# Kernel optimization log

Measured on AMD Instinct MI355X. Metric: run time of the kernel, lower is better.

The kernel has to match this reference:

```python
import jax, jax.numpy as jnp
import numpy as np
from jax import lax

# Mamba2 hyperparameters (mamba_ssm defaults scaled to d_model=512)
D_MODEL = 512
EXPAND = 2
D_INNER = EXPAND * D_MODEL          # 1024
HEADDIM = 64
NHEADS = D_INNER // HEADDIM         # 16
D_STATE = 64
NGROUPS = 1
D_CONV = 4
CONV_DIM = D_INNER + 2 * NGROUPS * D_STATE   # 1152
D_IN_PROJ = 2 * D_INNER + 2 * NGROUPS * D_STATE + NHEADS  # 2192
EPS = 1e-5


def setup_inputs() -> dict:
    key = jax.random.key(0)
    ks = jax.random.split(key, 8)
    x = jax.random.normal(ks[0], (4, 2044, D_MODEL), jnp.float32)
    in_proj_w = jax.random.normal(ks[1], (D_MODEL, D_IN_PROJ), jnp.float32) * 0.02
    conv_w = jax.random.normal(ks[2], (CONV_DIM, 1, D_CONV), jnp.float32) * 0.2  # depthwise [O,I/g,K]
    conv_b = jnp.zeros((CONV_DIM,), jnp.float32)
    dt_bias = jax.random.uniform(ks[3], (NHEADS,), jnp.float32, 0.0, 0.1)
    A_log = jnp.log(jax.random.uniform(ks[4], (NHEADS,), jnp.float32, 1.0, 16.0))
    D_skip = jnp.ones((NHEADS,), jnp.float32)
    norm_w = jnp.ones((D_INNER,), jnp.float32)
    out_proj_w = jax.random.normal(ks[5], (D_INNER, D_MODEL), jnp.float32) * 0.02
    return {
        "x": x, "in_proj_w": in_proj_w, "conv_w": conv_w, "conv_b": conv_b,
        "dt_bias": dt_bias, "A_log": A_log, "D_skip": D_skip,
        "norm_w": norm_w, "out_proj_w": out_proj_w,
    }


def _mamba2(x, in_proj_w, conv_w, conv_b, dt_bias, A_log, D_skip, norm_w, out_proj_w):
    B, Lp, _ = x.shape
    zxbcdt = x @ in_proj_w                                  # [B,Lp,D_IN_PROJ]
    z = zxbcdt[..., :D_INNER]                               # gate
    xBC = zxbcdt[..., D_INNER:D_INNER + CONV_DIM]
    dt = zxbcdt[..., D_INNER + CONV_DIM:]                   # [B,Lp,H]

    # causal depthwise conv over time, then silu
    xBC_c = lax.conv_general_dilated(
        xBC.transpose(0, 2, 1), conv_w, window_strides=(1,),
        padding=[(D_CONV - 1, 0)], feature_group_count=CONV_DIM,
        dimension_numbers=("NCH", "OIH", "NCH"))
    xBC = jax.nn.silu(xBC_c.transpose(0, 2, 1) + conv_b)    # [B,Lp,CONV_DIM]

    xs = xBC[..., :D_INNER]
    Bm = xBC[..., D_INNER:D_INNER + NGROUPS * D_STATE]      # [B,Lp,N] (g=1)
    Cm = xBC[..., D_INNER + NGROUPS * D_STATE:]             # [B,Lp,N]

    dt = jax.nn.softplus(dt + dt_bias)                      # [B,Lp,H]
    A = -jnp.exp(A_log)                                     # [H]
    xh = xs.reshape(B, Lp, NHEADS, HEADDIM)                 # [B,Lp,H,P]

    decay = jnp.exp(dt * A)                                 # [B,Lp,H]
    dtx = dt[..., None] * xh                                # [B,Lp,H,P]

    def step(h, inp):
        dec_t, dtx_t, B_t, C_t = inp                        # [B,H],[B,H,P],[B,N],[B,N]
        h = dec_t[:, :, None, None] * h + dtx_t[..., None] * B_t[:, None, None, :]
        y_t = jnp.einsum("bhpn,bn->bhp", h, C_t)
        return h, y_t

    h0 = jnp.zeros((B, NHEADS, HEADDIM, D_STATE), x.dtype)
    _, ys = lax.scan(step, h0, (decay.transpose(1, 0, 2),
                                dtx.transpose(1, 0, 2, 3),
                                Bm.transpose(1, 0, 2),
                                Cm.transpose(1, 0, 2)))
    y = ys.transpose(1, 0, 2, 3) + D_skip[None, None, :, None] * xh  # [B,Lp,H,P]
    y = y.reshape(B, Lp, D_INNER)

    # gated RMSNorm (RMSNormGated): gate first, then normalize
    y = y * jax.nn.silu(z)
    y = y * lax.rsqrt(jnp.mean(y * y, axis=-1, keepdims=True) + EPS) * norm_w
    return y @ out_proj_w                                   # [B,Lp,D_MODEL]


def reference(x, in_proj_w, conv_w, conv_b, dt_bias, A_log, D_skip, norm_w, out_proj_w):
    # MemoryEfficientMamba wrapper: pad seq_len to multiple of 8, run mamba, slice back
    L = x.shape[1]
    pad = (-L) % 8
    xp = jnp.pad(x, ((0, 0), (0, pad), (0, 0))) if pad else x
    out = _mamba2(xp, in_proj_w, conv_w, conv_b, dt_bias, A_log, D_skip, norm_w, out_proj_w)
    return out[:, :L, :]
```

## Files before the change

kernel.cpp:

```cpp
#include <hip/hip_runtime.h>
#include <hip/hip_bf16.h>
#include <math.h>
#include <string.h>

#define BATCH   4
#define SEQ     2044
#define DMODEL  512
#define DINNER  1024
#define NHEADS  16
#define HEADDIM 64
#define DSTATE  64
#define CONVDIM 1152
#define DINPROJ 2192
#define ZW      2176
#define NROWS   (BATCH*SEQ)
#define Q       64
#define NCHUNK  32

typedef __attribute__((ext_vector_type(8))) short bf16x8;
typedef __attribute__((ext_vector_type(4))) float f32x4;

#define MFMA(a,b,c) __builtin_amdgcn_mfma_f32_16x16x32_bf16((a),(b),(c),0,0,0)

__device__ inline short f2bf(float f) {
    __hip_bfloat16 h = __float2bfloat16(f);
    short s; memcpy(&s, &h, 2); return s;
}
__device__ inline float bf2f(short s) {
    unsigned u = ((unsigned)(unsigned short)s) << 16;
    float f; memcpy(&f, &u, 4); return f;
}

__device__ __forceinline__ void gload16(const short* g, short* l) {
    __builtin_amdgcn_global_load_lds(
        (const __attribute__((address_space(1))) void*)g,
        (__attribute__((address_space(3))) void*)l, 16, 0, 0);
}

__global__ __launch_bounds__(256) void convert_bf16_kernel(const float* __restrict__ in,
                                                           short* __restrict__ out, int n8) {
    int i = blockIdx.x * 256 + threadIdx.x;
    if (i >= n8) return;
    float4 v0 = *((const float4*)in + i * 2);
    float4 v1 = *((const float4*)in + i * 2 + 1);
    short t[8];
    t[0]=f2bf(v0.x); t[1]=f2bf(v0.y); t[2]=f2bf(v0.z); t[3]=f2bf(v0.w);
    t[4]=f2bf(v1.x); t[5]=f2bf(v1.y); t[6]=f2bf(v1.z); t[7]=f2bf(v1.w);
    *((bf16x8*)out + i) = *(const bf16x8*)t;
}

__global__ __launch_bounds__(256) void transpose_cvt_kernel(const float* __restrict__ in,
                                                            short* __restrict__ out,
                                                            int R, int Cc, int ldi) {
    __shared__ float tile[64][65];
    const int bx = blockIdx.x * 64;
    const int by = blockIdx.y * 64;
    const int tid = threadIdx.x;
#pragma unroll
    for (int i = 0; i < 16; i++) {
        int idx = tid + i * 256; int r = idx >> 6, c = idx & 63;
        float v = 0.f;
        if (by + r < R && bx + c < Cc) v = in[(size_t)(by + r) * ldi + bx + c];
        tile[r][c] = v;
    }
    __syncthreads();
#pragma unroll
    for (int i = 0; i < 16; i++) {
        int idx = tid + i * 256; int c = idx >> 6, r = idx & 63;
        if (bx + c < Cc && by + r < R)
            out[(size_t)(bx + c) * R + by + r] = f2bf(tile[r][c]);
    }
}

template<bool BF16OUT>
__global__ __launch_bounds__(256) void gemm_bf16(const short* __restrict__ A,
                                                 const short* __restrict__ Bt,
                                                 void* __restrict__ Cv,
                                                 int M, int N, int K,
                                                 int Nbf, float* __restrict__ dtout,
                                                 const float* __restrict__ dt_bias,
                                                 const float* __restrict__ A_log) {
    __shared__ short As[2][64][64];
    __shared__ short Bs[2][64][64];
    const int tid = threadIdx.x;
    const int wave = tid >> 6, lane = tid & 63;
    const int bm = blockIdx.x * 64, bn = blockIdx.y * 64;
    const int lane15 = lane & 15;
    const int kgrp = lane >> 4;
    const int srow = lane >> 3;
    const int scol = (lane & 7) ^ srow;
    const int r7 = lane15 & 7;

    f32x4 acc[4];
#pragma unroll
    for (int j = 0; j < 4; j++) acc[j] = (f32x4){0.f, 0.f, 0.f, 0.f};

    const short* Ab = A + (size_t)(bm + wave * 16 + srow) * K + scol * 8;
    const short* Bb = Bt + (size_t)(bn + wave * 16 + srow) * K + scol * 8;

    gload16(Ab,                 &As[0][wave * 16][0]);
    gload16(Ab + 8 * (size_t)K, &As[0][wave * 16 + 8][0]);
    gload16(Bb,                 &Bs[0][wave * 16][0]);
    gload16(Bb + 8 * (size_t)K, &Bs[0][wave * 16 + 8][0]);
    __syncthreads();

    const int nk = K >> 6;
    int cur = 0;
    for (int s = 0; s < nk; s++) {
        if (s + 1 < nk) {
            const int kk = (s + 1) << 6;
            const int nxt = cur ^ 1;
            gload16(Ab + kk,                 &As[nxt][wave * 16][0]);
            gload16(Ab + 8 * (size_t)K + kk, &As[nxt][wave * 16 + 8][0]);
            gload16(Bb + kk,                 &Bs[nxt][wave * 16][0]);
            gload16(Bb + 8 * (size_t)K + kk, &Bs[nxt][wave * 16 + 8][0]);
        }
        const int arow = (wave << 4) + lane15;
        bf16x8 a0 = *(const bf16x8*)&As[cur][arow][(kgrp ^ r7) * 8];
        bf16x8 a1 = *(const bf16x8*)&As[cur][arow][((kgrp + 4) ^ r7) * 8];
#pragma unroll
        for (int j = 0; j < 4; j++) {
            const int brow = (j << 4) + lane15;
            bf16x8 b0 = *(const bf16x8*)&Bs[cur][brow][(kgrp ^ r7) * 8];
            bf16x8 b1 = *(const bf16x8*)&Bs[cur][brow][((kgrp + 4) ^ r7) * 8];
            acc[j] = MFMA(a0, b0, acc[j]);
            acc[j] = MFMA(a1, b1, acc[j]);
        }
        __syncthreads();
        cur ^= 1;
    }

    const int crow = bm + (wave << 4) + ((lane >> 4) << 2);
    const int ccol0 = bn + lane15;
    const int ndt = N - Nbf;
#pragma unroll
    for (int j = 0; j < 4; j++) {
        int gn = ccol0 + j * 16;
        if (gn >= N) continue;
#pragma unroll
        for (int i = 0; i < 4; i++) {
            int gm = crow + i;
            if (gm >= M) continue;
            float v = acc[j][i];
            if (BF16OUT) {
                if (dtout != nullptr && gn >= Nbf) {
                    int h = gn - Nbf;
                    float v2 = v + dt_bias[h];
                    float sp = (v2 > 20.f) ? v2 : log1pf(expf(v2));
                    dtout[(size_t)gm * ndt + h] = sp * (-expf(A_log[h]));
                } else {
                    ((short*)Cv)[(size_t)gm * Nbf + gn] = f2bf(v);
                }
            } else {
                ((float*)Cv)[(size_t)gm * N + gn] = v;
            }
        }
    }
}

__global__ __launch_bounds__(256) void conv_silu_kernel(const short* __restrict__ zxb,
                                                        const float* __restrict__ conv_w,
                                                        const float* __restrict__ conv_b,
                                                        short* __restrict__ convo) {
    int idx = blockIdx.x * 256 + threadIdx.x;
    if (idx >= BATCH * (SEQ/4) * CONVDIM) return;
    int c = idx % CONVDIM;
    int q = idx / CONVDIM;
    int b = q / (SEQ/4);
    int t0 = (q % (SEQ/4)) * 4;
    const size_t base = ((size_t)b * SEQ + t0) * ZW + DINNER + c;
    float4 wv = *(const float4*)&conv_w[c * 4];
    float xv[7];
#pragma unroll
    for (int i = 0; i < 7; i++) {
        int t = t0 - 3 + i;
        xv[i] = (t >= 0) ? bf2f(zxb[base + (size_t)(i - 3) * ZW]) : 0.f;
    }
    const float bias = conv_b[c];
    const size_t obase = ((size_t)b * SEQ + t0) * CONVDIM + c;
#pragma unroll
    for (int i = 0; i < 4; i++) {
        float a = bias + xv[i]*wv.x + xv[i+1]*wv.y + xv[i+2]*wv.z + xv[i+3]*wv.w;
        float s = a / (1.f + expf(-a));
        convo[obase + (size_t)i * CONVDIM] = f2bf(s);
    }
}

__global__ __launch_bounds__(256) void chunk_state_kernel(
    const short* __restrict__ convo,
    const float* __restrict__ lab,
    const float* __restrict__ A_log,
    short* __restrict__ Sbf,
    float* __restrict__ atot)
{
    const int blk = blockIdx.x;
    const int h  = blk & 15;
    const int bc = blk >> 4;
    const int c  = bc & (NCHUNK - 1);
    const int b  = bc >> 5;
    const int t0 = c * Q;
    const int len = min(Q, SEQ - t0);
    const int tid = threadIdx.x;
    const int wave = tid >> 6, lane = tid & 63;
    const size_t rowbase = (size_t)b * SEQ + t0;

    __shared__ short Xt[64][72];
    __shared__ short Bw[64][72];
    __shared__ float sw[64];

    if (tid < 64) {
        const float nAinv = -expf(-A_log[h]);
        float lav = 0.f;
        if (tid < len) lav = lab[(rowbase + tid) * NHEADS + h];
        float dtv = lav * nAinv;
        float v = lav;
#pragma unroll
        for (int off = 1; off < 64; off <<= 1) {
            float nb = __shfl_up(v, off);
            if (lane >= off) v += nb;
        }
        float last = __shfl(v, 63);
        sw[tid] = expf(last - v) * dtv;
        if (tid == 63) atot[blk] = expf(last);
    }
    __syncthreads();

    {
        const int r = tid >> 2, qq = tid & 3;
        const bf16x8 zz = {0,0,0,0,0,0,0,0};
        bf16x8 b0 = zz, b1 = zz, x0 = zz, x1 = zz;
        if (r < len) {
            const short* row = convo + (rowbase + r) * CONVDIM;
            b0 = *(const bf16x8*)&row[1024 + qq*16];
            b1 = *(const bf16x8*)&row[1024 + qq*16 + 8];
            x0 = *(const bf16x8*)&row[h*64 + qq*16];
            x1 = *(const bf16x8*)&row[h*64 + qq*16 + 8];
        }
        const float wsc = sw[r];
        short bs[16], xs[16];
        *(bf16x8*)&bs[0] = b0; *(bf16x8*)&bs[8] = b1;
        *(bf16x8*)&xs[0] = x0; *(bf16x8*)&xs[8] = x1;
#pragma unroll
        for (int i = 0; i < 16; i++) Xt[qq*16+i][r] = xs[i];
#pragma unroll
        for (int i = 0; i < 16; i++) Bw[qq*16+i][r] = f2bf(bf2f(bs[i]) * wsc);
    }
    __syncthreads();

    const int arow = (wave << 4) + (lane & 15);
    const int koff = (lane >> 4) << 3;
    const int trow0 = (wave << 4) + ((lane >> 4) << 2);
    const int scol = lane & 15;

    f32x4 sacc[4];
#pragma unroll
    for (int j = 0; j < 4; j++) sacc[j] = (f32x4){0.f,0.f,0.f,0.f};
    {
        bf16x8 a0 = *(const bf16x8*)&Xt[arow][koff];
        bf16x8 a1 = *(const bf16x8*)&Xt[arow][32 + koff];
#pragma unroll
        for (int j = 0; j < 4; j++) {
            const int brow = (j << 4) + (lane & 15);
            bf16x8 b0 = *(const bf16x8*)&Bw[brow][koff];
            bf16x8 b1 = *(const bf16x8*)&Bw[brow][32 + koff];
            sacc[j] = MFMA(a0, b0, sacc[j]);
            sacc[j] = MFMA(a1, b1, sacc[j]);
        }
    }
    const size_t sbase = (size_t)blk * 4096;
#pragma unroll
    for (int j = 0; j < 4; j++) {
        int n = j * 16 + scol;
#pragma unroll
        for (int i = 0; i < 4; i++) {
            int p = trow0 + i;
            Sbf[sbase + p * 64 + n] = f2bf(sacc[j][i]);
        }
    }
}

__global__ __launch_bounds__(256) void chunk_state_scan_kernel(
    const short* __restrict__ Sbf, const float* __restrict__ atot,
    short* __restrict__ Hbf)
{
    int e = blockIdx.x * 256 + threadIdx.x;
    int bh = e >> 12;
    int el = e & 4095;
    int b = bh >> 4, h = bh & 15;
    float H = 0.f;
    for (int c = 0; c < NCHUNK; c++) {
        int blk = (b * NCHUNK + c) * NHEADS + h;
        size_t off = (size_t)blk * 4096 + el;
        Hbf[off] = f2bf(H);
        H = atot[blk] * H + bf2f(Sbf[off]);
    }
}

__global__ __launch_bounds__(256) void chunk_yfuse_kernel(
    const short* __restrict__ convo,
    const float* __restrict__ lab,
    const float* __restrict__ A_log,
    const float* __restrict__ D_skip,
    const short* __restrict__ Hbf,
    short* __restrict__ ybf)
{
    const int blk = blockIdx.x;
    const int h  = blk & 15;
    const int bc = blk >> 4;
    const int c  = bc & (NCHUNK - 1);
    const int b  = bc >> 5;
    const int t0 = c * Q;
    const int len = min(Q, SEQ - t0);
    const int tid = threadIdx.x;
    const int wave = tid >> 6, lane = tid & 63;
    const size_t rowbase = (size_t)b * SEQ + t0;

    __shared__ short Ct[64][72];
    __shared__ short Bt2[64][72];
    __shared__ short Xt[64][72];
    __shared__ short Hs[64][72];
    __shared__ float cum[64], sdt[64];

    if (tid < 64) {
        const float nAinv = -expf(-A_log[h]);
        float lav = 0.f;
        if (tid < len) lav = lab[(rowbase + tid) * NHEADS + h];
        float dtv = lav * nAinv;
        float v = lav;
#pragma unroll
        for (int off = 1; off < 64; off <<= 1) {
            float nb = __shfl_up(v, off);
            if (lane >= off) v += nb;
        }
        cum[tid] = v; sdt[tid] = dtv;
    }
    __syncthreads();

    {
        const int r = tid >> 2, qq = tid & 3;
        const bf16x8 zz = {0,0,0,0,0,0,0,0};
        bf16x8 c0 = zz, c1 = zz, b0 = zz, b1 = zz, x0 = zz, x1 = zz;
        if (r < len) {
            const short* row = convo + (rowbase + r) * CONVDIM;
            c0 = *(const bf16x8*)&row[1088 + qq*16];
            c1 = *(const bf16x8*)&row[1088 + qq*16 + 8];
            b0 = *(const bf16x8*)&row[1024 + qq*16];
            b1 = *(const bf16x8*)&row[1024 + qq*16 + 8];
            x0 = *(const bf16x8*)&row[h*64 + qq*16];
            x1 = *(const bf16x8*)&row[h*64 + qq*16 + 8];
        }
        *(bf16x8*)&Ct[r][qq*16]    = c0; *(bf16x8*)&Ct[r][qq*16+8]  = c1;
        *(bf16x8*)&Bt2[r][qq*16]   = b0; *(bf16x8*)&Bt2[r][qq*16+8] = b1;
        short xs[16];
        *(bf16x8*)&xs[0] = x0; *(bf16x8*)&xs[8] = x1;
#pragma unroll
        for (int i = 0; i < 16; i++) Xt[qq*16+i][r] = xs[i];
        const size_t hbase = (size_t)blk * 4096;
        bf16x8 h0 = *(const bf16x8*)&Hbf[hbase + r*64 + qq*16];
        bf16x8 h1 = *(const bf16x8*)&Hbf[hbase + r*64 + qq*16 + 8];
        *(bf16x8*)&Hs[r][qq*16]   = h0;
        *(bf16x8*)&Hs[r][qq*16+8] = h1;
    }
    __syncthreads();

    const int arow = (wave << 4) + (lane & 15);
    const int koff = (lane >> 4) << 3;
    const int trow0 = (wave << 4) + ((lane >> 4) << 2);
    const int scol = lane & 15;

    f32x4 eacc[4], iacc[4];
#pragma unroll
    for (int j = 0; j < 4; j++) { eacc[j] = (f32x4){0.f,0.f,0.f,0.f}; iacc[j] = (f32x4){0.f,0.f,0.f,0.f}; }
    {
        bf16x8 a0 = *(const bf16x8*)&Ct[arow][koff];
        bf16x8 a1 = *(const bf16x8*)&Ct[arow][32 + koff];
#pragma unroll
        for (int j = 0; j < 4; j++) {
            const int brow = (j << 4) + (lane & 15);
            bf16x8 b0 = *(const bf16x8*)&Bt2[brow][koff];
            bf16x8 b1 = *(const bf16x8*)&Bt2[brow][32 + koff];
            eacc[j] = MFMA(a0, b0, eacc[j]);
            eacc[j] = MFMA(a1, b1, eacc[j]);
            bf16x8 h0 = *(const bf16x8*)&Hs[brow][koff];
            bf16x8 h1 = *(const bf16x8*)&Hs[brow][32 + koff];
            iacc[j] = MFMA(a0, h0, iacc[j]);
            iacc[j] = MFMA(a1, h1, iacc[j]);
        }
    }
    short ebf[4][4];
#pragma unroll
    for (int j = 0; j < 4; j++) {
        int s = j * 16 + scol;
#pragma unroll
        for (int i = 0; i < 4; i++) {
            int t = trow0 + i;
            float val = 0.f;
            if (s <= t) val = eacc[j][i] * expf(cum[t] - cum[s]) * sdt[s];
            ebf[j][i] = f2bf(val);
        }
    }
    __syncthreads();
#pragma unroll
    for (int j = 0; j < 4; j++)
#pragma unroll
        for (int i = 0; i < 4; i++)
            Ct[trow0 + i][j * 16 + scol] = ebf[j][i];
    __syncthreads();

    f32x4 yacc[4];
#pragma unroll
    for (int j = 0; j < 4; j++) yacc[j] = (f32x4){0.f,0.f,0.f,0.f};
    {
        bf16x8 a0 = *(const bf16x8*)&Ct[arow][koff];
        bf16x8 a1 = *(const bf16x8*)&Ct[arow][32 + koff];
#pragma unroll
        for (int j = 0; j < 4; j++) {
            const int brow = (j << 4) + (lane & 15);
            bf16x8 b0 = *(const bf16x8*)&Xt[brow][koff];
            bf16x8 b1 = *(const bf16x8*)&Xt[brow][32 + koff];
            yacc[j] = MFMA(a0, b0, yacc[j]);
            yacc[j] = MFMA(a1, b1, yacc[j]);
        }
    }
    const float dsk = D_skip[h];
#pragma unroll
    for (int j = 0; j < 4; j++) {
        int p = j * 16 + scol;
#pragma unroll
        for (int i = 0; i < 4; i++) {
            int t = trow0 + i;
            if (t < len) {
                float ce = expf(cum[t]);
                float xv = bf2f(Xt[p][t]);
                float val = yacc[j][i] + ce * iacc[j][i] + dsk * xv;
                ybf[(rowbase + t) * DINNER + h * 64 + p] = f2bf(val);
            }
        }
    }
}

__global__ __launch_bounds__(256) void gate_rmsnorm_kernel(short* __restrict__ y,
                                                           const short* __restrict__ zxb,
                                                           const float* __restrict__ norm_w) {
    const int m = blockIdx.x;
    const int tid = threadIdx.x;
    float vals[4];
    float ss = 0.f;
#pragma unroll
    for (int i = 0; i < 4; i++) {
        int c = tid + i * 256;
        float v = bf2f(y[(size_t)m * DINNER + c]);
        float z = bf2f(zxb[(size_t)m * ZW + c]);
        float g = v * (z / (1.f + expf(-z)));
        vals[i] = g;
        ss += g * g;
    }
#pragma unroll
    for (int mask = 1; mask < 64; mask <<= 1) ss += __shfl_xor(ss, mask);
    __shared__ float red[4];
    if ((tid & 63) == 0) red[tid >> 6] = ss;
    __syncthreads();
    float tot = red[0] + red[1] + red[2] + red[3];
    float scale = rsqrtf(tot / 1024.f + 1e-5f);
#pragma unroll
    for (int i = 0; i < 4; i++) {
        int c = tid + i * 256;
        float r = vals[i] * scale * norm_w[c];
        y[(size_t)m * DINNER + c] = f2bf(r);
    }
}

extern "C" void kernel_launch(void* const* d_in, const int* in_sizes, int n_in,
                              void* d_out, int out_size, void* d_ws, size_t ws_size,
                              hipStream_t stream) {
    const float* x          = (const float*)d_in[0];
    const float* in_proj_w  = (const float*)d_in[1];
    const float* conv_w     = (const float*)d_in[2];
    const float* conv_b     = (const float*)d_in[3];
    const float* dt_bias    = (const float*)d_in[4];
    const float* A_log      = (const float*)d_in[5];
    const float* D_skip     = (const float*)d_in[6];
    const float* norm_w     = (const float*)d_in[7];
    const float* out_proj_w = (const float*)d_in[8];
    float* out = (float*)d_out;

    short* zxb   = (short*)d_ws;
    short* convo = zxb + (size_t)NROWS * ZW;
    short* ybf   = convo + (size_t)NROWS * CONVDIM;
    short* Hbf   = ybf + (size_t)NROWS * DINNER;
    short* Sbf   = Hbf + (size_t)2048 * 4096;
    float* lab   = (float*)(Sbf + (size_t)2048 * 4096);
    float* atotb = lab + (size_t)NROWS * NHEADS;
    short* w2t   = (short*)(atotb + 2048);
    short* xb  = convo;
    short* w1t = xb + (size_t)NROWS * DMODEL;

    convert_bf16_kernel<<<(NROWS * DMODEL / 8 + 255) / 256, 256, 0, stream>>>(x, xb, NROWS * DMODEL / 8);
    {
        dim3 g((DINPROJ + 63) / 64, (DMODEL + 63) / 64);
        transpose_cvt_kernel<<<g, 256, 0, stream>>>(in_proj_w, w1t, DMODEL, DINPROJ, DINPROJ);
    }
    {
        dim3 g((DMODEL + 63) / 64, (DINNER + 63) / 64);
        transpose_cvt_kernel<<<g, 256, 0, stream>>>(out_proj_w, w2t, DINNER, DMODEL, DMODEL);
    }

    {
        dim3 g((NROWS + 63) / 64, (DINPROJ + 63) / 64);
        gemm_bf16<true><<<g, 256, 0, stream>>>(xb, w1t, zxb, NROWS, DINPROJ, DMODEL,
                                               ZW, lab, dt_bias, A_log);
    }

    {
        int tot = BATCH * (SEQ / 4) * CONVDIM;
        conv_silu_kernel<<<(tot + 255) / 256, 256, 0, stream>>>(zxb, conv_w, conv_b, convo);
    }

    chunk_state_kernel<<<BATCH * NCHUNK * NHEADS, 256, 0, stream>>>(
        convo, lab, A_log, Sbf, atotb);

    chunk_state_scan_kernel<<<(64 * 4096) / 256, 256, 0, stream>>>(Sbf, atotb, Hbf);

    chunk_yfuse_kernel<<<BATCH * NCHUNK * NHEADS, 256, 0, stream>>>(
        convo, lab, A_log, D_skip, Hbf, ybf);

    gate_rmsnorm_kernel<<<NROWS, 256, 0, stream>>>(ybf, zxb, norm_w);

    {
        dim3 g((NROWS + 63) / 64, (DMODEL + 63) / 64);
        gemm_bf16<false><<<g, 256, 0, stream>>>(ybf, w2t, out, NROWS, DMODEL, DINNER,
                                                DMODEL, nullptr, nullptr, nullptr);
    }
}
```

Baseline: 149.5 us.

## Enlarge GEMM tile to 128x64 and drop LDS double buffering

The bf16 GEMM block tile grows from 64x64 to 128x64. Each wave now computes a 32x64 sub-tile with 2x4 accumulators, so every B fragment loaded from LDS feeds two MFMA rows. The double-buffered shared-memory pipeline is replaced by a single buffer with load, sync, compute, sync per k-step. This cuts redundant B traffic and halves the block count, but it loses the overlap of global loads with compute and raises register pressure.

```diff
diff --git a/kernel.cpp b/kernel.cpp
--- a/kernel.cpp
+++ b/kernel.cpp
@@ -80,79 +80,82 @@
                                                  int Nbf, float* __restrict__ dtout,
                                                  const float* __restrict__ dt_bias,
                                                  const float* __restrict__ A_log) {
-    __shared__ short As[2][64][64];
-    __shared__ short Bs[2][64][64];
+    __shared__ short As[128][64];
+    __shared__ short Bs[64][64];
     const int tid = threadIdx.x;
     const int wave = tid >> 6, lane = tid & 63;
-    const int bm = blockIdx.x * 64, bn = blockIdx.y * 64;
+    const int bm = blockIdx.x * 128, bn = blockIdx.y * 64;
     const int lane15 = lane & 15;
     const int kgrp = lane >> 4;
     const int srow = lane >> 3;
     const int scol = (lane & 7) ^ srow;
     const int r7 = lane15 & 7;
 
-    f32x4 acc[4];
-#pragma unroll
-    for (int j = 0; j < 4; j++) acc[j] = (f32x4){0.f, 0.f, 0.f, 0.f};
-
-    const short* Ab = A + (size_t)(bm + wave * 16 + srow) * K + scol * 8;
+    f32x4 acc[2][4];
+#pragma unroll
+    for (int i = 0; i < 2; i++)
+#pragma unroll
+        for (int j = 0; j < 4; j++) acc[i][j] = (f32x4){0.f, 0.f, 0.f, 0.f};
+
+    const short* Ab = A + (size_t)(bm + wave * 32 + srow) * K + scol * 8;
     const short* Bb = Bt + (size_t)(bn + wave * 16 + srow) * K + scol * 8;
 
-    gload16(Ab,                 &As[0][wave * 16][0]);
-    gload16(Ab + 8 * (size_t)K, &As[0][wave * 16 + 8][0]);
-    gload16(Bb,                 &Bs[0][wave * 16][0]);
-    gload16(Bb + 8 * (size_t)K, &Bs[0][wave * 16 + 8][0]);
-    __syncthreads();
-
-    const int nk = K >> 6;
-    int cur = 0;
-    for (int s = 0; s < nk; s++) {
-        if (s + 1 < nk) {
-            const int kk = (s + 1) << 6;
-            const int nxt = cur ^ 1;
-            gload16(Ab + kk,                 &As[nxt][wave * 16][0]);
-            gload16(Ab + 8 * (size_t)K + kk, &As[nxt][wave * 16 + 8][0]);
-            gload16(Bb + kk,                 &Bs[nxt][wave * 16][0]);
-            gload16(Bb + 8 * (size_t)K + kk, &Bs[nxt][wave * 16 + 8][0]);
-        }
-        const int arow = (wave << 4) + lane15;
-        bf16x8 a0 = *(const bf16x8*)&As[cur][arow][(kgrp ^ r7) * 8];
-        bf16x8 a1 = *(const bf16x8*)&As[cur][arow][((kgrp + 4) ^ r7) * 8];
+    for (int kk = 0; kk < K; kk += 64) {
+        gload16(Ab + kk,                  &As[wave * 32][0]);
+        gload16(Ab + 8  * (size_t)K + kk, &As[wave * 32 + 8][0]);
+        gload16(Ab + 16 * (size_t)K + kk, &As[wave * 32 + 16][0]);
+        gload16(Ab + 24 * (size_t)K + kk, &As[wave * 32 + 24][0]);
+        gload16(Bb + kk,                  &Bs[wave * 16][0]);
+        gload16(Bb + 8  * (size_t)K + kk, &Bs[wave * 16 + 8][0]);
+        __syncthreads();
+        bf16x8 af[2][2], bfm[4][2];
+#pragma unroll
+        for (int i = 0; i < 2; i++) {
+            int ar = wave * 32 + i * 16 + lane15;
+            af[i][0] = *(const bf16x8*)&As[ar][(kgrp ^ r7) * 8];
+            af[i][1] = *(const bf16x8*)&As[ar][((kgrp + 4) ^ r7) * 8];
+        }
 #pragma unroll
         for (int j = 0; j < 4; j++) {
-            const int brow = (j << 4) + lane15;
-            bf16x8 b0 = *(const bf16x8*)&Bs[cur][brow][(kgrp ^ r7) * 8];
-            bf16x8 b1 = *(const bf16x8*)&Bs[cur][brow][((kgrp + 4) ^ r7) * 8];
-            acc[j] = MFMA(a0, b0, acc[j]);
-            acc[j] = MFMA(a1, b1, acc[j]);
-        }
+            int br = (j << 4) + lane15;
+            bfm[j][0] = *(const bf16x8*)&Bs[br][(kgrp ^ r7) * 8];
+            bfm[j][1] = *(const bf16x8*)&Bs[br][((kgrp + 4) ^ r7) * 8];
+        }
+#pragma unroll
+        for (int i = 0; i < 2; i++)
+#pragma unroll
+            for (int j = 0; j < 4; j++) {
+                acc[i][j] = MFMA(af[i][0], bfm[j][0], acc[i][j]);
+                acc[i][j] = MFMA(af[i][1], bfm[j][1], acc[i][j]);
+            }
         __syncthreads();
-        cur ^= 1;
-    }
-
-    const int crow = bm + (wave << 4) + ((lane >> 4) << 2);
-    const int ccol0 = bn + lane15;
+    }
+
+    const int rbase = (lane >> 4) << 2;
     const int ndt = N - Nbf;
 #pragma unroll
     for (int j = 0; j < 4; j++) {
-        int gn = ccol0 + j * 16;
+        int gn = bn + j * 16 + lane15;
         if (gn >= N) continue;
 #pragma unroll
-        for (int i = 0; i < 4; i++) {
-            int gm = crow + i;
-            if (gm >= M) continue;
-            float v = acc[j][i];
-            if (BF16OUT) {
-                if (dtout != nullptr && gn >= Nbf) {
-                    int h = gn - Nbf;
-                    float v2 = v + dt_bias[h];
-                    float sp = (v2 > 20.f) ? v2 : log1pf(expf(v2));
-                    dtout[(size_t)gm * ndt + h] = sp * (-expf(A_log[h]));
+        for (int i = 0; i < 2; i++) {
+#pragma unroll
+            for (int reg = 0; reg < 4; reg++) {
+                int gm = bm + wave * 32 + i * 16 + rbase + reg;
+                if (gm >= M) continue;
+                float v = acc[i][j][reg];
+                if (BF16OUT) {
+                    if (dtout != nullptr && gn >= Nbf) {
+                        int h = gn - Nbf;
+                        float v2 = v + dt_bias[h];
+                        float sp = (v2 > 20.f) ? v2 : log1pf(expf(v2));
+                        dtout[(size_t)gm * ndt + h] = sp * (-expf(A_log[h]));
+                    } else {
+                        ((short*)Cv)[(size_t)gm * Nbf + gn] = f2bf(v);
+                    }
                 } else {
-                    ((short*)Cv)[(size_t)gm * Nbf + gn] = f2bf(v);
+                    ((float*)Cv)[(size_t)gm * N + gn] = v;
                 }
-            } else {
-                ((float*)Cv)[(size_t)gm * N + gn] = v;
             }
         }
     }
@@ -506,7 +509,7 @@
     }
 
     {
-        dim3 g((NROWS + 63) / 64, (DINPROJ + 63) / 64);
+        dim3 g((NROWS + 127) / 128, (DINPROJ + 63) / 64);
         gemm_bf16<true><<<g, 256, 0, stream>>>(xb, w1t, zxb, NROWS, DINPROJ, DMODEL,
                                                ZW, lab, dt_bias, A_log);
     }
@@ -527,7 +530,7 @@
     gate_rmsnorm_kernel<<<NROWS, 256, 0, stream>>>(ybf, zxb, norm_w);
 
     {
-        dim3 g((NROWS + 63) / 64, (DMODEL + 63) / 64);
+        dim3 g((NROWS + 127) / 128, (DMODEL + 63) / 64);
         gemm_bf16<false><<<g, 256, 0, stream>>>(ybf, w2t, out, NROWS, DMODEL, DINNER,
                                                 DMODEL, nullptr, nullptr, nullptr);
     }
```

New measurement: 142.1 us. -4.9%, faster.
